# Kernel optimization log

Hardware: AMD Instinct MI355X
Metric: run time of the kernel (lower is better)

## Reference

```python
import jax, jax.numpy as jnp
import numpy as np

B, S, H, NH, L, FF, V, T = 16, 256, 768, 12, 12, 3072, 30522, 9
DH = H // NH
LN_EPS = 1e-12


def _ln(x, g, b):
    m = jnp.mean(x, axis=-1, keepdims=True)
    v = jnp.mean((x - m) ** 2, axis=-1, keepdims=True)
    return (x - m) * jax.lax.rsqrt(v + LN_EPS) * g + b


def setup_inputs():
    key = jax.random.key(0)
    ks = jax.random.split(key, 20)
    n = lambda i, shape: jax.random.normal(ks[i], shape, jnp.float32) * 0.02
    lengths = jax.random.randint(ks[0], (B,), S // 2, S + 1)
    attention_mask = (jnp.arange(S)[None, :] < lengths[:, None]).astype(jnp.int32)
    return {
        "input_ids": jax.random.randint(ks[1], (B, S), 0, V),
        "attention_mask": attention_mask,
        "labels": jax.random.randint(ks[2], (B, S), 0, T),
        "word_emb": n(3, (V, H)),
        "pos_emb": n(4, (512, H)),
        "type_emb": n(5, (2, H)),
        "emb_g": jnp.ones((H,), jnp.float32), "emb_b": jnp.zeros((H,), jnp.float32),
        "lWq": n(6, (L, H, H)), "lbq": jnp.zeros((L, H), jnp.float32),
        "lWk": n(7, (L, H, H)), "lbk": jnp.zeros((L, H), jnp.float32),
        "lWv": n(8, (L, H, H)), "lbv": jnp.zeros((L, H), jnp.float32),
        "lWo": n(9, (L, H, H)), "lbo": jnp.zeros((L, H), jnp.float32),
        "lg1": jnp.ones((L, H), jnp.float32), "lb1": jnp.zeros((L, H), jnp.float32),
        "lWi": n(10, (L, H, FF)), "lbi": jnp.zeros((L, FF), jnp.float32),
        "lWf": n(11, (L, FF, H)), "lbf": jnp.zeros((L, H), jnp.float32),
        "lg2": jnp.ones((L, H), jnp.float32), "lb2": jnp.zeros((L, H), jnp.float32),
        "cls_W": n(12, (H, T)), "cls_b": jnp.zeros((T,), jnp.float32),
        "crf_start": jax.random.uniform(ks[13], (T,), jnp.float32, -0.1, 0.1),
        "crf_end": jax.random.uniform(ks[14], (T,), jnp.float32, -0.1, 0.1),
        "crf_trans": jax.random.uniform(ks[15], (T, T), jnp.float32, -0.1, 0.1),
    }


def _encoder(input_ids, attention_mask, word_emb, pos_emb, type_emb, emb_g, emb_b, layer_stack, cls_W, cls_b):
    x = word_emb[input_ids] + pos_emb[:S][None] + type_emb[0][None, None]  # [B,S,H]
    x = _ln(x, emb_g, emb_b)
    bias = (1.0 - attention_mask.astype(jnp.float32))[:, None, None, :] * -1e9  # [B,1,1,S]
    scale = 1.0 / np.sqrt(DH).astype(np.float32)

    def layer(h, p):
        Wq, bq, Wk, bk, Wv, bv, Wo, bo, g1, b1, Wi, bi, Wf, bf, g2, b2 = p
        q = (h @ Wq + bq).reshape(B, S, NH, DH)
        k = (h @ Wk + bk).reshape(B, S, NH, DH)
        v = (h @ Wv + bv).reshape(B, S, NH, DH)
        att = jax.nn.softmax(jnp.einsum('bqhd,bkhd->bhqk', q, k) * scale + bias, axis=-1)
        ctx = jnp.einsum('bhqk,bkhd->bqhd', att, v).reshape(B, S, H)
        h = _ln(h + ctx @ Wo + bo, g1, b1)
        ff = jax.nn.gelu(h @ Wi + bi, approximate=False) @ Wf + bf
        h = _ln(h + ff, g2, b2)
        return h, None

    x, _ = jax.lax.scan(layer, x, layer_stack)
    return x @ cls_W + cls_b  # [B,S,T]


def _crf_llh(em, tg, m, start, end, trans):
    # pytorch-crf forward, reduction='sum'. em [B,Lc,T], tg [B,Lc] int, m [B,Lc] bool
    mf = m.astype(em.dtype)
    em_sc = jnp.take_along_axis(em, tg[..., None], axis=-1)[..., 0]  # [B,Lc]
    tr_sc = trans[tg[:, :-1], tg[:, 1:]]                             # [B,Lc-1]
    num = start[tg[:, 0]] + em_sc[:, 0] + jnp.sum(mf[:, 1:] * (tr_sc + em_sc[:, 1:]), axis=1)
    seq_ends = jnp.sum(m.astype(jnp.int32), axis=1) - 1
    last_tag = jnp.take_along_axis(tg, seq_ends[:, None], axis=1)[:, 0]
    num = num + end[last_tag]

    def step(score, xs):
        em_t, m_t = xs
        nxt = jax.nn.logsumexp(score[:, :, None] + trans[None] + em_t[:, None, :], axis=1)
        return jnp.where(m_t[:, None], nxt, score), None

    score0 = start[None] + em[:, 0]
    score, _ = jax.lax.scan(step, score0, (em[:, 1:].transpose(1, 0, 2), m[:, 1:].transpose(1, 0)))
    den = jax.nn.logsumexp(score + end[None], axis=1)
    return jnp.sum(num - den)


def _viterbi(em, start, end, trans):
    # decode over the FULL sequence with all-ones mask (matches crf.decode(logits))
    def step(score, em_t):
        cand = score[:, :, None] + trans[None] + em_t[:, None, :]  # [B,T,T]
        return jnp.max(cand, axis=1), jnp.argmax(cand, axis=1)

    score0 = start[None] + em[:, 0]
    score, hist = jax.lax.scan(step, score0, em[:, 1:].transpose(1, 0, 2))  # hist [S-1,B,T]
    last = jnp.argmax(score + end[None], axis=1)  # [B]

    def back(tag, h):
        prev = jnp.take_along_axis(h, tag[:, None], axis=1)[:, 0]
        return prev, prev

    _, rev = jax.lax.scan(back, last, hist, reverse=True)  # rev[i] = tag at time i, i in [0,S-2]
    tags = jnp.concatenate([rev.transpose(1, 0), last[:, None]], axis=1)  # [B,S]
    return tags.astype(jnp.float32)


def reference(input_ids, attention_mask, labels, word_emb, pos_emb, type_emb, emb_g, emb_b,
              lWq, lbq, lWk, lbk, lWv, lbv, lWo, lbo, lg1, lb1, lWi, lbi, lWf, lbf, lg2, lb2,
              cls_W, cls_b, crf_start, crf_end, crf_trans):
    layer_stack = (lWq, lbq, lWk, lbk, lWv, lbv, lWo, lbo, lg1, lb1, lWi, lbi, lWf, lbf, lg2, lb2)
    logits = _encoder(input_ids, attention_mask, word_emb, pos_emb, type_emb, emb_g, emb_b, layer_stack, cls_W, cls_b)
    str_lens = jnp.sum(attention_mask, axis=-1)
    pos = jnp.arange(S)[None, :]
    mask = attention_mask.astype(bool) & (pos > 0) & (pos != (str_lens - 1)[:, None])
    tags_in = jnp.where(mask, labels, jnp.zeros_like(labels))
    loss = -_crf_llh(logits[:, 1:], tags_in[:, 1:], mask[:, 1:], crf_start, crf_end, crf_trans)
    tags = _viterbi(logits, crf_start, crf_end, crf_trans)
    return (loss, tags)
```

## Files before the change

### kernel.cpp

```cpp
#include <hip/hip_runtime.h>

#define B_ 16
#define S_ 256
#define H_ 768
#define NH_ 12
#define DH_ 64
#define L_ 12
#define FF_ 3072
#define T_ 9
#define NTOK (B_*S_)

#define AS1 __attribute__((address_space(1)))
#define AS3 __attribute__((address_space(3)))

typedef __attribute__((ext_vector_type(8))) short bfrag;
typedef __attribute__((ext_vector_type(8))) unsigned short us8;
typedef __attribute__((ext_vector_type(4))) float f4;

#define LOG2E_ 1.4426950408889634f
#define LN2_   0.6931471805599453f

__device__ inline unsigned short f2bf(float x) {
    unsigned u = __builtin_bit_cast(unsigned, x);
    return (unsigned short)((u + 0x7fffu + ((u >> 16) & 1u)) >> 16);
}
__device__ inline float bf2f(unsigned short h) {
    unsigned u = ((unsigned)h) << 16;
    return __builtin_bit_cast(float, u);
}
__device__ inline void pack8(const float* v, us8& h, us8& l) {
    #pragma unroll
    for (int j = 0; j < 8; j++) {
        unsigned short hh = f2bf(v[j]);
        h[j] = hh;
        l[j] = f2bf(v[j] - bf2f(hh));
    }
}

__global__ __launch_bounds__(256) void k_conv_w(
    const float* __restrict__ Wq, const float* __restrict__ Wk,
    const float* __restrict__ Wv, const float* __restrict__ Wo,
    const float* __restrict__ Wi, const float* __restrict__ Wf,
    const float* __restrict__ bq, const float* __restrict__ bk, const float* __restrict__ bv,
    float* __restrict__ qkvbias, unsigned short* __restrict__ Wpk)
{
    int bid = blockIdx.x;
    int tid = threadIdx.x;
    if (bid == 0) {
        for (int i = tid; i < 3 * H_; i += 256)
            qkvbias[i] = (i < H_) ? bq[i] : (i < 2 * H_) ? bk[i - H_] : bv[i - 2 * H_];
    }
    const float* src; int Kd, Nd; size_t doff; int t;
    if (bid < 576)       { int m = bid / 144; src = (m == 0) ? Wq : (m == 1) ? Wk : (m == 2) ? Wv : Wo;
                           Kd = H_; Nd = H_; doff = (size_t)m * 73728; t = bid % 144; }
    else if (bid < 1152) { src = Wi; Kd = H_; Nd = FF_; doff = 294912; t = bid - 576; }
    else                 { src = Wf; Kd = FF_; Nd = H_; doff = 589824; t = bid - 1152; }
    int ntn = Nd / 64;
    int tk = t / ntn, tn = t % ntn;
    int k0 = tk * 64, n0 = tn * 64;
    __shared__ float tile[64][65];
    int r = tid >> 6, c = tid & 63;
    #pragma unroll
    for (int i = 0; i < 16; i++)
        tile[r + i * 4][c] = src[(size_t)(k0 + r + i * 4) * Nd + n0 + c];
    __syncthreads();
    #pragma unroll
    for (int e = 0; e < 2; e++) {
        int item = tid * 2 + e;
        int nl = item >> 3, kb = item & 7;
        float v8[8];
        #pragma unroll
        for (int j = 0; j < 8; j++) v8[j] = tile[kb * 8 + j][nl];
        us8 h, l; pack8(v8, h, l);
        unsigned short* p = Wpk + (doff + (size_t)(n0 + nl) * (Kd / 8) + (k0 / 8 + kb)) * 16;
        *reinterpret_cast<us8*>(p) = h;
        *reinterpret_cast<us8*>(p + 8) = l;
    }
}

__global__ __launch_bounds__(128) void k_embed_ln(
    const int* __restrict__ ids, const float* __restrict__ wemb,
    const float* __restrict__ pemb, const float* __restrict__ temb,
    const float* __restrict__ g, const float* __restrict__ bb,
    unsigned short* __restrict__ out_pk)
{
    int tok = blockIdx.x;
    int s = tok & (S_ - 1);
    int id = ids[tok];
    int tid = threadIdx.x;
    bool act = tid < 96;
    int idx = tid * 8;
    float v8[8];
    float sum = 0.f;
    if (act) {
        const float4* w4 = reinterpret_cast<const float4*>(wemb + (size_t)id * H_ + idx);
        const float4* p4 = reinterpret_cast<const float4*>(pemb + (size_t)s * H_ + idx);
        const float4* t4 = reinterpret_cast<const float4*>(temb + idx);
        #pragma unroll
        for (int q = 0; q < 2; q++) {
            float4 a = w4[q], b = p4[q], c = t4[q];
            v8[q*4+0] = a.x + b.x + c.x; v8[q*4+1] = a.y + b.y + c.y;
            v8[q*4+2] = a.z + b.z + c.z; v8[q*4+3] = a.w + b.w + c.w;
        }
        #pragma unroll
        for (int j = 0; j < 8; j++) sum += v8[j];
    }
    __shared__ float wsum[2], wvar[2];
    #pragma unroll
    for (int o = 32; o > 0; o >>= 1) sum += __shfl_xor(sum, o);
    if ((tid & 63) == 0) wsum[tid >> 6] = sum;
    __syncthreads();
    float mean = (wsum[0] + wsum[1]) * (1.0f / H_);
    float vs = 0.f;
    if (act) {
        for (int j = 0; j < 8; j++) { float d = v8[j] - mean; vs += d * d; }
    }
    #pragma unroll
    for (int o = 32; o > 0; o >>= 1) vs += __shfl_xor(vs, o);
    if ((tid & 63) == 0) wvar[tid >> 6] = vs;
    __syncthreads();
    float inv = 1.0f / sqrtf((wvar[0] + wvar[1]) * (1.0f / H_) + 1e-12f);
    if (act) {
        float o8[8];
        #pragma unroll
        for (int j = 0; j < 8; j++) o8[j] = (v8[j] - mean) * inv * g[idx + j] + bb[idx + j];
        us8 h, l; pack8(o8, h, l);
        unsigned short* p = out_pk + ((size_t)tok * 96 + tid) * 16;
        *reinterpret_cast<us8*>(p) = h;
        *reinterpret_cast<us8*>(p + 8) = l;
    }
}

__global__ __launch_bounds__(128) void k_res_ln(
    const float* __restrict__ x, const float* __restrict__ g, const float* __restrict__ bb,
    unsigned short* __restrict__ h_pk)
{
    int tok = blockIdx.x;
    int tid = threadIdx.x;
    bool act = tid < 96;
    int idx = tid * 8;
    float v8[8];
    float sum = 0.f;
    unsigned short* p = h_pk + ((size_t)tok * 96 + tid) * 16;
    if (act) {
        const float4* x4 = reinterpret_cast<const float4*>(x + (size_t)tok * H_ + idx);
        us8 hi = *reinterpret_cast<const us8*>(p);
        us8 lo = *reinterpret_cast<const us8*>(p + 8);
        float4 a0 = x4[0], a1 = x4[1];
        float xs[8] = {a0.x, a0.y, a0.z, a0.w, a1.x, a1.y, a1.z, a1.w};
        #pragma unroll
        for (int j = 0; j < 8; j++) {
            v8[j] = xs[j] + bf2f(hi[j]) + bf2f(lo[j]);
            sum += v8[j];
        }
    }
    __shared__ float wsum[2], wvar[2];
    #pragma unroll
    for (int o = 32; o > 0; o >>= 1) sum += __shfl_xor(sum, o);
    if ((tid & 63) == 0) wsum[tid >> 6] = sum;
    __syncthreads();
    float mean = (wsum[0] + wsum[1]) * (1.0f / H_);
    float vs = 0.f;
    if (act) {
        for (int j = 0; j < 8; j++) { float d = v8[j] - mean; vs += d * d; }
    }
    #pragma unroll
    for (int o = 32; o > 0; o >>= 1) vs += __shfl_xor(vs, o);
    if ((tid & 63) == 0) wvar[tid >> 6] = vs;
    __syncthreads();
    float inv = 1.0f / sqrtf((wvar[0] + wvar[1]) * (1.0f / H_) + 1e-12f);
    if (act) {
        float o8[8];
        #pragma unroll
        for (int j = 0; j < 8; j++) o8[j] = (v8[j] - mean) * inv * g[idx + j] + bb[idx + j];
        us8 h, l; pack8(o8, h, l);
        *reinterpret_cast<us8*>(p) = h;
        *reinterpret_cast<us8*>(p + 8) = l;
    }
}

__global__ __launch_bounds__(256) void k_gemm_pk(
    const unsigned short* __restrict__ A, const unsigned short* __restrict__ Wp,
    const float* __restrict__ bias,
    float* __restrict__ C0, float* __restrict__ C1, float* __restrict__ C2, int cpb,
    unsigned short* __restrict__ Cpk,
    int M, int N, int K, int act, int cbx)
{
    constexpr int BUFSZ = 24576;
    __shared__ char smem[3 * BUFSZ];
    unsigned smb = (unsigned)(size_t)(void*)smem;

    int id = blockIdx.x;
    int xcd = id & 7;
    int rr = id >> 3;
    int by = (xcd >> 1) * 8 + rr / cbx;
    int bx = (xcd & 1) * cbx + rr % cbx;
    int m0 = by << 7, n0 = bx << 6;
    int Kb = K >> 3;
    int nst = Kb >> 2;
    int rowbytes = Kb * 32;

    int tid = threadIdx.x;
    int lane = tid & 63, wid = tid >> 6;
    int wm = wid >> 1, wn = wid & 1;
    int fr = lane & 15, fq = lane >> 4;

    f4 acc[4][2];
    #pragma unroll
    for (int i = 0; i < 4; i++)
        #pragma unroll
        for (int j = 0; j < 2; j++) acc[i][j] = (f4){0.f, 0.f, 0.f, 0.f};

    const char* agp[4];
    const char* bgp[2];
    #pragma unroll
    for (int i = 0; i < 4; i++) {
        int d = i * 4096 + tid * 16;
        int row = d >> 7;
        int colp = (d & 127) ^ ((row & 7) << 4);
        agp[i] = (const char*)A + (size_t)(m0 + row) * rowbytes + colp;
    }
    #pragma unroll
    for (int i = 0; i < 2; i++) {
        int d = i * 4096 + tid * 16;
        int row = d >> 7;
        int colp = (d & 127) ^ ((row & 7) << 4);
        bgp[i] = (const char*)Wp + (size_t)(n0 + row) * rowbytes + colp;
    }

    int afo[4], bfo[2];
    #pragma unroll
    for (int mi = 0; mi < 4; mi++) {
        int r = wm * 64 + mi * 16 + fr;
        afo[mi] = r * 128 + ((fq * 32) ^ ((r & 7) << 4));
    }
    #pragma unroll
    for (int ni = 0; ni < 2; ni++) {
        int rb = wn * 32 + ni * 16 + fr;
        bfo[ni] = 16384 + rb * 128 + ((fq * 32) ^ ((rb & 7) << 4));
    }

    auto issue = [&](int ks, unsigned boff) {
        size_t ko = (size_t)ks * 128;
        #pragma unroll
        for (int i = 0; i < 4; i++)
            __builtin_amdgcn_global_load_lds((const AS1 void*)(size_t)(agp[i] + ko),
                (AS3 void*)(unsigned)(smb + boff + i * 4096 + wid * 1024), 16, 0, 0);
        #pragma unroll
        for (int i = 0; i < 2; i++)
            __builtin_amdgcn_global_load_lds((const AS1 void*)(size_t)(bgp[i] + ko),
                (AS3 void*)(unsigned)(smb + boff + 16384 + i * 4096 + wid * 1024), 16, 0, 0);
    };

    issue(0, 0);
    if (nst > 1) issue(1, BUFSZ);
    unsigned c0 = 0, c1 = BUFSZ, c2 = 2 * BUFSZ;

    for (int ks = 0; ks < nst; ks++) {
        if (ks + 1 < nst) asm volatile("s_waitcnt vmcnt(6)" ::: "memory");
        else              asm volatile("s_waitcnt vmcnt(0)" ::: "memory");
        __builtin_amdgcn_s_barrier();
        __builtin_amdgcn_sched_barrier(0);
        if (ks + 2 < nst) issue(ks + 2, c2);

        const char* cbp = smem + c0;
        bfrag ah[4], al[4], bh[2], bl[2];
        #pragma unroll
        for (int mi = 0; mi < 4; mi++) {
            ah[mi] = *reinterpret_cast<const bfrag*>(cbp + afo[mi]);
            al[mi] = *reinterpret_cast<const bfrag*>(cbp + (afo[mi] ^ 16));
        }
        #pragma unroll
        for (int ni = 0; ni < 2; ni++) {
            bh[ni] = *reinterpret_cast<const bfrag*>(cbp + bfo[ni]);
            bl[ni] = *reinterpret_cast<const bfrag*>(cbp + (bfo[ni] ^ 16));
        }
        #pragma unroll
        for (int mi = 0; mi < 4; mi++) {
            #pragma unroll
            for (int ni = 0; ni < 2; ni++) {
                acc[mi][ni] = __builtin_amdgcn_mfma_f32_16x16x32_bf16(ah[mi], bh[ni], acc[mi][ni], 0, 0, 0);
                acc[mi][ni] = __builtin_amdgcn_mfma_f32_16x16x32_bf16(ah[mi], bl[ni], acc[mi][ni], 0, 0, 0);
                acc[mi][ni] = __builtin_amdgcn_mfma_f32_16x16x32_bf16(al[mi], bh[ni], acc[mi][ni], 0, 0, 0);
            }
        }
        unsigned t = c0; c0 = c1; c1 = c2; c2 = t;
    }

    if (act == 0) {
        #pragma unroll
        for (int mi = 0; mi < 4; mi++) {
            #pragma unroll
            for (int ni = 0; ni < 2; ni++) {
                int col = n0 + wn * 32 + ni * 16 + fr;
                float bv = bias[col];
                int buf = col / cpb;
                float* Cp = (buf == 0) ? C0 : (buf == 1) ? C1 : C2;
                int cc = col - buf * cpb;
                #pragma unroll
                for (int r = 0; r < 4; r++) {
                    int row = m0 + wm * 64 + mi * 16 + fq * 4 + r;
                    Cp[(size_t)row * cpb + cc] = acc[mi][ni][r] + bv;
                }
            }
        }
    } else {
        __syncthreads();
        float* ebuf = (float*)(smem + wid * 2432);
        int Nb = N >> 3;
        #pragma unroll
        for (int mi = 0; mi < 4; mi++) {
            #pragma unroll
            for (int ni = 0; ni < 2; ni++) {
                int col = n0 + wn * 32 + ni * 16 + fr;
                float bv = bias[col];
                #pragma unroll
                for (int r = 0; r < 4; r++) {
                    float v = acc[mi][ni][r] + bv;
                    v = 0.5f * v * (1.0f + erff(v * 0.70710678118654752f));
                    ebuf[(fq * 4 + r) * 38 + ni * 16 + fr] = v;
                }
            }
            int row16 = lane >> 2, kb = lane & 3;
            float v8[8];
            #pragma unroll
            for (int j = 0; j < 8; j++) v8[j] = ebuf[row16 * 38 + kb * 8 + j];
            us8 h, l; pack8(v8, h, l);
            int grow = m0 + wm * 64 + mi * 16 + row16;
            int gcb = ((n0 + wn * 32) >> 3) + kb;
            unsigned short* p = Cpk + ((size_t)grow * Nb + gcb) * 16;
            *reinterpret_cast<us8*>(p) = h;
            *reinterpret_cast<us8*>(p + 8) = l;
        }
    }
}

#define SM_KH 0
#define SM_KL 5632
#define SM_VH 11264
#define SM_VL 16384
#define SM_PH 21504
#define SM_PL 26624
__global__ __launch_bounds__(256) void k_attn_fused(
    const float* __restrict__ Q, const float* __restrict__ Kb,
    const float* __restrict__ V, const int* __restrict__ amask,
    unsigned short* __restrict__ ctx_pk)
{
    __shared__ char smem[31744];
    unsigned short* KhS = (unsigned short*)(smem + SM_KH);
    unsigned short* KlS = (unsigned short*)(smem + SM_KL);
    unsigned short* VhS = (unsigned short*)(smem + SM_VH);
    unsigned short* VlS = (unsigned short*)(smem + SM_VL);
    unsigned short* PhS = (unsigned short*)(smem + SM_PH);
    unsigned short* PlS = (unsigned short*)(smem + SM_PL);

    int idx = blockIdx.x;
    int qt = idx & 3;
    int hd = (idx >> 2) % NH_;
    int b = idx / (4 * NH_);
    int tid = threadIdx.x;
    int lane = tid & 63, wid = tid >> 6;
    int fr = lane & 15, fq = lane >> 4;

    int q0 = qt * 64 + wid * 16;

    bfrag qh[2], ql[2];
    {
        const float* qbase = Q + ((size_t)(b * S_ + q0 + fr)) * H_ + hd * DH_;
        #pragma unroll
        for (int ks = 0; ks < 2; ks++) {
            const float4* p = reinterpret_cast<const float4*>(qbase + ks * 32 + fq * 8);
            float4 v0 = p[0], v1 = p[1];
            float vv[8] = {v0.x, v0.y, v0.z, v0.w, v1.x, v1.y, v1.z, v1.w};
            #pragma unroll
            for (int j = 0; j < 8; j++) {
                unsigned short h = f2bf(vv[j]);
                qh[ks][j] = (short)h;
                ql[ks][j] = (short)f2bf(vv[j] - bf2f(h));
            }
        }
    }

    f4 o[4];
    #pragma unroll
    for (int i = 0; i < 4; i++) o[i] = (f4){0.f, 0.f, 0.f, 0.f};
    float m[4], l[4];
    #pragma unroll
    for (int r = 0; r < 4; r++) { m[r] = -3e38f; l[r] = 0.f; }

    int kvrow = tid >> 3;
    int dbase = (tid & 7) * 8;

    for (int t = 0; t < 8; t++) {
        {
            const float* src = Kb + ((size_t)(b * S_ + t * 32 + kvrow)) * H_ + hd * DH_ + dbase;
            float4 a4 = reinterpret_cast<const float4*>(src)[0];
            float4 b4 = reinterpret_cast<const float4*>(src)[1];
            float vv[8] = {a4.x, a4.y, a4.z, a4.w, b4.x, b4.y, b4.z, b4.w};
            us8 h, l2;
            #pragma unroll
            for (int j = 0; j < 8; j++) {
                unsigned short hh = f2bf(vv[j]);
                h[j] = hh; l2[j] = f2bf(vv[j] - bf2f(hh));
            }
            *reinterpret_cast<us8*>(&KhS[kvrow * 88 + dbase]) = h;
            *reinterpret_cast<us8*>(&KlS[kvrow * 88 + dbase]) = l2;
        }
        {
            const float* src = V + ((size_t)(b * S_ + t * 32 + kvrow)) * H_ + hd * DH_ + dbase;
            float4 a4 = reinterpret_cast<const float4*>(src)[0];
            float4 b4 = reinterpret_cast<const float4*>(src)[1];
            float vv[8] = {a4.x, a4.y, a4.z, a4.w, b4.x, b4.y, b4.z, b4.w};
            #pragma unroll
            for (int j = 0; j < 8; j++) {
                unsigned short h = f2bf(vv[j]);
                VhS[(dbase + j) * 40 + kvrow] = h;
                VlS[(dbase + j) * 40 + kvrow] = f2bf(vv[j] - bf2f(h));
            }
        }
        __syncthreads();

        f4 s0 = (f4){0.f,0.f,0.f,0.f}, s1 = (f4){0.f,0.f,0.f,0.f};
        #pragma unroll
        for (int ks = 0; ks < 2; ks++) {
            bfrag kbh0 = *reinterpret_cast<const bfrag*>(&KhS[fr * 88 + ks * 32 + fq * 8]);
            bfrag kbl0 = *reinterpret_cast<const bfrag*>(&KlS[fr * 88 + ks * 32 + fq * 8]);
            bfrag kbh1 = *reinterpret_cast<const bfrag*>(&KhS[(16 + fr) * 88 + ks * 32 + fq * 8]);
            bfrag kbl1 = *reinterpret_cast<const bfrag*>(&KlS[(16 + fr) * 88 + ks * 32 + fq * 8]);
            s0 = __builtin_amdgcn_mfma_f32_16x16x32_bf16(qh[ks], kbh0, s0, 0, 0, 0);
            s0 = __builtin_amdgcn_mfma_f32_16x16x32_bf16(qh[ks], kbl0, s0, 0, 0, 0);
            s0 = __builtin_amdgcn_mfma_f32_16x16x32_bf16(ql[ks], kbh0, s0, 0, 0, 0);
            s1 = __builtin_amdgcn_mfma_f32_16x16x32_bf16(qh[ks], kbh1, s1, 0, 0, 0);
            s1 = __builtin_amdgcn_mfma_f32_16x16x32_bf16(qh[ks], kbl1, s1, 0, 0, 0);
            s1 = __builtin_amdgcn_mfma_f32_16x16x32_bf16(ql[ks], kbh1, s1, 0, 0, 0);
        }

        float cb0 = (amask[b * S_ + t * 32 + fr] == 0) ? -1e9f : 0.f;
        float cb1 = (amask[b * S_ + t * 32 + 16 + fr] == 0) ? -1e9f : 0.f;
        float sc0[4], sc1[4], fct[4], pr0[4], pr1[4];
        #pragma unroll
        for (int r = 0; r < 4; r++) {
            sc0[r] = s0[r] * 0.125f + cb0;
            sc1[r] = s1[r] * 0.125f + cb1;
            float tm = fmaxf(sc0[r], sc1[r]);
            #pragma unroll
            for (int od = 1; od < 16; od <<= 1) tm = fmaxf(tm, __shfl_xor(tm, od));
            float mn = fmaxf(m[r], tm);
            fct[r] = expf(m[r] - mn);
            pr0[r] = expf(sc0[r] - mn);
            pr1[r] = expf(sc1[r] - mn);
            float rs = pr0[r] + pr1[r];
            #pragma unroll
            for (int od = 1; od < 16; od <<= 1) rs += __shfl_xor(rs, od);
            l[r] = l[r] * fct[r] + rs;
            m[r] = mn;
        }
        #pragma unroll
        for (int ci = 0; ci < 4; ci++)
            #pragma unroll
            for (int r = 0; r < 4; r++) o[ci][r] *= fct[r];

        #pragma unroll
        for (int r = 0; r < 4; r++) {
            int row = fq * 4 + r;
            unsigned short h0 = f2bf(pr0[r]);
            PhS[wid * 640 + row * 40 + fr] = h0;
            PlS[wid * 640 + row * 40 + fr] = f2bf(pr0[r] - bf2f(h0));
            unsigned short h1 = f2bf(pr1[r]);
            PhS[wid * 640 + row * 40 + 16 + fr] = h1;
            PlS[wid * 640 + row * 40 + 16 + fr] = f2bf(pr1[r] - bf2f(h1));
        }

        bfrag pah = *reinterpret_cast<const bfrag*>(&PhS[wid * 640 + fr * 40 + fq * 8]);
        bfrag pal = *reinterpret_cast<const bfrag*>(&PlS[wid * 640 + fr * 40 + fq * 8]);
        #pragma unroll
        for (int ci = 0; ci < 4; ci++) {
            bfrag vbh = *reinterpret_cast<const bfrag*>(&VhS[(ci * 16 + fr) * 40 + fq * 8]);
            bfrag vbl = *reinterpret_cast<const bfrag*>(&VlS[(ci * 16 + fr) * 40 + fq * 8]);
            o[ci] = __builtin_amdgcn_mfma_f32_16x16x32_bf16(pah, vbh, o[ci], 0, 0, 0);
            o[ci] = __builtin_amdgcn_mfma_f32_16x16x32_bf16(pah, vbl, o[ci], 0, 0, 0);
            o[ci] = __builtin_amdgcn_mfma_f32_16x16x32_bf16(pal, vbh, o[ci], 0, 0, 0);
        }
        __syncthreads();
    }

    __syncthreads();
    float* eb = (float*)smem + wid * 1088;
    #pragma unroll
    for (int r = 0; r < 4; r++) {
        float inv = 1.0f / l[r];
        #pragma unroll
        for (int ci = 0; ci < 4; ci++)
            eb[(fq * 4 + r) * 68 + ci * 16 + fr] = o[ci][r] * inv;
    }
    __syncthreads();
    #pragma unroll
    for (int e = 0; e < 2; e++) {
        int item = lane * 2 + e;
        int row16 = item >> 3, kb = item & 7;
        float v8[8];
        #pragma unroll
        for (int j = 0; j < 8; j++) v8[j] = eb[row16 * 68 + kb * 8 + j];
        us8 h, l2; pack8(v8, h, l2);
        int grow = b * S_ + q0 + row16;
        int gcb = hd * 8 + kb;
        unsigned short* p = ctx_pk + ((size_t)grow * 96 + gcb) * 16;
        *reinterpret_cast<us8*>(p) = h;
        *reinterpret_cast<us8*>(p + 8) = l2;
    }
}

__global__ __launch_bounds__(64) void k_classifier(
    const unsigned short* __restrict__ Hpk, const float* __restrict__ Wc,
    const float* __restrict__ bc, float* __restrict__ logits)
{
    int tok = blockIdx.x;
    int lane = threadIdx.x;
    float acc[T_];
    #pragma unroll
    for (int j = 0; j < T_; j++) acc[j] = 0.f;
    for (int kb = lane; kb < 96; kb += 64) {
        const unsigned short* p = Hpk + ((size_t)tok * 96 + kb) * 16;
        us8 hi = *reinterpret_cast<const us8*>(p);
        us8 lo = *reinterpret_cast<const us8*>(p + 8);
        #pragma unroll
        for (int e = 0; e < 8; e++) {
            float hv = bf2f(hi[e]) + bf2f(lo[e]);
            const float* wr = Wc + (size_t)(kb * 8 + e) * T_;
            #pragma unroll
            for (int j = 0; j < T_; j++) acc[j] = fmaf(hv, wr[j], acc[j]);
        }
    }
    #pragma unroll
    for (int j = 0; j < T_; j++) {
        float v = acc[j];
        for (int o = 32; o > 0; o >>= 1) v += __shfl_down(v, o);
        if (lane == 0) logits[(size_t)tok * T_ + j] = v + bc[j];
    }
}

__global__ __launch_bounds__(256) void k_crf_vit(
    const float* __restrict__ logits, const int* __restrict__ amask,
    const int* __restrict__ labels, const float* __restrict__ start,
    const float* __restrict__ endv, const float* __restrict__ trans,
    float* __restrict__ out)
{
    int blk = blockIdx.x;
    int tid = threadIdx.x;
    if (blk == 0) {
        __shared__ float res[B_];
        int lane = tid & 63;
        int bb = (tid >> 6) * 4 + (lane >> 4);
        int sj = lane & 15;
        int lb = lane & 48;

        int cnt = 0;
        for (int s = sj; s < S_; s += 16) cnt += amask[bb * S_ + s];
        #pragma unroll
        for (int o = 8; o > 0; o >>= 1) cnt += __shfl_xor(cnt, o);
        int len = cnt;
        int lim = len - 1;

        float num = 0.f;
        for (int s = 2 + sj; s < S_; s += 16) {
            if (s < lim) {
                int tp = labels[bb * S_ + s - 1];
                int tc = labels[bb * S_ + s];
                num += trans[tp * T_ + tc] + logits[((size_t)(bb * S_ + s)) * T_ + tc];
            }
        }
        #pragma unroll
        for (int o = 8; o > 0; o >>= 1) num += __shfl_xor(num, o);
        int tg1 = labels[bb * S_ + 1];
        num += start[tg1] + logits[((size_t)(bb * S_ + 1)) * T_ + tg1];
        num += endv[labels[bb * S_ + (len - 2)]];

        float tc9[T_];
        #pragma unroll
        for (int i = 0; i < T_; i++) tc9[i] = (sj < T_) ? trans[i * T_ + sj] * LOG2E_ : 0.f;
        float score = (sj < T_) ? (start[sj] + logits[((size_t)(bb * S_ + 1)) * T_ + sj]) * LOG2E_ : 0.f;
        float base = 0.f;
        const float* embase = logits + (size_t)bb * S_ * T_ + sj;
        float emb[8];
        #pragma unroll
        for (int c = 0; c < 8; c++) emb[c] = (sj < T_) ? embase[(2 + c) * T_] : 0.f;
        for (int s0 = 2; s0 < S_; s0 += 8) {
            #pragma unroll
            for (int c = 0; c < 8; c++) {
                int s = s0 + c;
                if (s < S_) {
                    float em = emb[c];
                    emb[c] = (sj < T_ && s + 8 < S_) ? embase[(size_t)(s + 8) * T_] : 0.f;
                    float si[T_];
                    #pragma unroll
                    for (int i = 0; i < T_; i++) si[i] = __shfl(score, lb + i);
                    float e2[T_];
                    #pragma unroll
                    for (int i = 0; i < T_; i++) e2[i] = exp2f(si[i] + tc9[i]);
                    float s01 = e2[0] + e2[1], s23 = e2[2] + e2[3];
                    float s45 = e2[4] + e2[5], s67 = e2[6] + e2[7];
                    float sum = ((s01 + s23) + (s45 + s67)) + e2[8];
                    float nsc = fmaf(em, LOG2E_, log2f(sum));
                    if (s < lim) score = nsc;
                }
            }
            float sh = __shfl(score, lb);
            score -= sh;
            base += sh;
        }
        float se = (sj < T_) ? score + endv[sj] * LOG2E_ : -1e30f;
        float fi[T_];
        #pragma unroll
        for (int i = 0; i < T_; i++) fi[i] = __shfl(se, lb + i);
        if (sj == 0) {
            float mx = -1e30f;
            #pragma unroll
            for (int i = 0; i < T_; i++) mx = fmaxf(mx, fi[i]);
            float sum = 0.f;
            #pragma unroll
            for (int i = 0; i < T_; i++) sum += exp2f(fi[i] - mx);
            res[bb] = (base + mx + log2f(sum)) * LN2_ - num;
        }
        __syncthreads();
        if (tid == 0) {
            float tot = 0.f;
            #pragma unroll
            for (int i = 0; i < B_; i++) tot += res[i];
            out[0] = tot;
        }
    } else {
        if (tid >= 64) return;
        int b = blk - 1;
        int j = tid;
        float* tags_out = out + 1;
        __shared__ unsigned char hist[S_ - 1][T_];
        float tc9[T_];
        #pragma unroll
        for (int i = 0; i < T_; i++) tc9[i] = (j < T_) ? trans[i * T_ + j] : 0.f;
        float score = (j < T_) ? start[j] + logits[((size_t)(b * S_)) * T_ + j] : -1e30f;
        const float* embase = logits + (size_t)b * S_ * T_ + j;
        float emb[8];
        #pragma unroll
        for (int c = 0; c < 8; c++) emb[c] = (j < T_) ? embase[(1 + c) * T_] : 0.f;
        for (int t0 = 1; t0 < S_; t0 += 8) {
            #pragma unroll
            for (int c = 0; c < 8; c++) {
                int t = t0 + c;
                if (t < S_) {
                    float em = emb[c];
                    emb[c] = (j < T_ && t + 8 < S_) ? embase[(size_t)(t + 8) * T_] : 0.f;
                    float si[T_];
                    #pragma unroll
                    for (int i = 0; i < T_; i++) si[i] = __shfl(score, i);
                    float cv[T_];
                    #pragma unroll
                    for (int i = 0; i < T_; i++) cv[i] = si[i] + tc9[i];
                    float v01 = cv[0]; int i01 = 0; if (cv[1] > v01) { v01 = cv[1]; i01 = 1; }
                    float v23 = cv[2]; int i23 = 2; if (cv[3] > v23) { v23 = cv[3]; i23 = 3; }
                    float v45 = cv[4]; int i45 = 4; if (cv[5] > v45) { v45 = cv[5]; i45 = 5; }
                    float v67 = cv[6]; int i67 = 6; if (cv[7] > v67) { v67 = cv[7]; i67 = 7; }
                    float v03 = v01; int i03 = i01; if (v23 > v03) { v03 = v23; i03 = i23; }
                    float v47 = v45; int i47 = i45; if (v67 > v47) { v47 = v67; i47 = i67; }
                    float v07 = v03; int i07 = i03; if (v47 > v07) { v07 = v47; i07 = i47; }
                    float best = v07; int bi = i07; if (cv[8] > best) { best = cv[8]; bi = 8; }
                    if (j < T_) {
                        hist[t - 1][j] = (unsigned char)bi;
                        score = best + em;
                    }
                }
            }
        }
        float se = (j < T_) ? score + endv[j] : -1e30f;
        float fi[T_];
        #pragma unroll
        for (int i = 0; i < T_; i++) fi[i] = __shfl(se, i);
        if (j == 0) {
            float best = -1e30f; int last = 0;
            #pragma unroll
            for (int i = 0; i < T_; i++) if (fi[i] > best) { best = fi[i]; last = i; }
            tags_out[b * S_ + (S_ - 1)] = (float)last;
            int cur = last;
            for (int t = S_ - 2; t >= 0; t--) {
                cur = hist[t][cur];
                tags_out[b * S_ + t] = (float)cur;
            }
        }
    }
}

extern "C" void kernel_launch(void* const* d_in, const int* in_sizes, int n_in,
                              void* d_out, int out_size, void* d_ws, size_t ws_size,
                              hipStream_t stream)
{
    const int*   input_ids = (const int*)d_in[0];
    const int*   amask     = (const int*)d_in[1];
    const int*   labels    = (const int*)d_in[2];
    const float* word_emb  = (const float*)d_in[3];
    const float* pos_emb   = (const float*)d_in[4];
    const float* type_emb  = (const float*)d_in[5];
    const float* emb_g     = (const float*)d_in[6];
    const float* emb_b     = (const float*)d_in[7];
    const float* lWq = (const float*)d_in[8];
    const float* lbq = (const float*)d_in[9];
    const float* lWk = (const float*)d_in[10];
    const float* lbk = (const float*)d_in[11];
    const float* lWv = (const float*)d_in[12];
    const float* lbv = (const float*)d_in[13];
    const float* lWo = (const float*)d_in[14];
    const float* lbo = (const float*)d_in[15];
    const float* lg1 = (const float*)d_in[16];
    const float* lb1 = (const float*)d_in[17];
    const float* lWi = (const float*)d_in[18];
    const float* lbi = (const float*)d_in[19];
    const float* lWf = (const float*)d_in[20];
    const float* lbf = (const float*)d_in[21];
    const float* lg2 = (const float*)d_in[22];
    const float* lb2 = (const float*)d_in[23];
    const float* cls_W = (const float*)d_in[24];
    const float* cls_b = (const float*)d_in[25];
    const float* crf_start = (const float*)d_in[26];
    const float* crf_end   = (const float*)d_in[27];
    const float* crf_trans = (const float*)d_in[28];

    float* out = (float*)d_out;
    float* ws = (float*)d_ws;

    const size_t NH32 = (size_t)NTOK * H_;
    float* h_pk_f  = ws + NH32;
    float* q       = ws + 2 * NH32;
    float* kbuf    = ws + 3 * NH32;
    float* v       = ws + 4 * NH32;
    float* ctxpk_f = ws + 5 * NH32;
    float* tmp     = ws + 6 * NH32;
    float* Wpk_f   = ws + 7 * NH32;
    float* qkvbias = Wpk_f + 7077888;
    float* logits  = qkvbias + 3 * H_;

    unsigned short* h_pk   = (unsigned short*)h_pk_f;
    unsigned short* ctx_pk = (unsigned short*)ctxpk_f;
    unsigned short* Wpk    = (unsigned short*)Wpk_f;
    unsigned short* big_pk = (unsigned short*)q;

    k_embed_ln<<<NTOK, 128, 0, stream>>>(input_ids, word_emb, pos_emb, type_emb, emb_g, emb_b, h_pk);

    const size_t WOFF_O = 221184, WOFF_I = 294912, WOFF_F = 589824;

    for (int l = 0; l < L_; l++) {
        k_conv_w<<<1728, 256, 0, stream>>>(
            lWq + (size_t)l * H_ * H_, lWk + (size_t)l * H_ * H_,
            lWv + (size_t)l * H_ * H_, lWo + (size_t)l * H_ * H_,
            lWi + (size_t)l * H_ * FF_, lWf + (size_t)l * FF_ * H_,
            lbq + (size_t)l * H_, lbk + (size_t)l * H_, lbv + (size_t)l * H_,
            qkvbias, Wpk);

        k_gemm_pk<<<1152, 256, 0, stream>>>(h_pk, Wpk, qkvbias,
            q, kbuf, v, H_, nullptr, NTOK, 3 * H_, H_, 0, 18);

        k_attn_fused<<<B_ * NH_ * 4, 256, 0, stream>>>(q, kbuf, v, amask, ctx_pk);

        k_gemm_pk<<<384, 256, 0, stream>>>(ctx_pk, Wpk + WOFF_O * 16, lbo + (size_t)l * H_,
            tmp, tmp, tmp, H_, nullptr, NTOK, H_, H_, 0, 6);

        k_res_ln<<<NTOK, 128, 0, stream>>>(tmp, lg1 + (size_t)l * H_, lb1 + (size_t)l * H_, h_pk);

        k_gemm_pk<<<1536, 256, 0, stream>>>(h_pk, Wpk + WOFF_I * 16, lbi + (size_t)l * FF_,
            tmp, tmp, tmp, FF_, big_pk, NTOK, FF_, H_, 1, 24);

        k_gemm_pk<<<384, 256, 0, stream>>>(big_pk, Wpk + WOFF_F * 16, lbf + (size_t)l * H_,
            tmp, tmp, tmp, H_, nullptr, NTOK, H_, FF_, 0, 6);

        k_res_ln<<<NTOK, 128, 0, stream>>>(tmp, lg2 + (size_t)l * H_, lb2 + (size_t)l * H_, h_pk);
    }

    k_classifier<<<NTOK, 64, 0, stream>>>(h_pk, cls_W, cls_b, logits);
    k_crf_vit<<<1 + B_, 256, 0, stream>>>(logits, amask, labels, crf_start, crf_end, crf_trans, out);
}
```

Before: 3.570 ms.

## Add 256x128 GEMM tile kernel for QKV/FFN-up and stage CRF emissions in LDS

```diff
diff --git a/kernel.cpp b/kernel.cpp
--- a/kernel.cpp
+++ b/kernel.cpp
@@ -179,12 +179,171 @@
     }
 }
 
-__global__ __launch_bounds__(256) void k_gemm_pk(
+__global__ __launch_bounds__(512) void k_gemm_big(
     const unsigned short* __restrict__ A, const unsigned short* __restrict__ Wp,
     const float* __restrict__ bias,
     float* __restrict__ C0, float* __restrict__ C1, float* __restrict__ C2, int cpb,
     unsigned short* __restrict__ Cpk,
     int M, int N, int K, int act, int cbx)
+{
+    constexpr int BUFSZ = 49152;
+    __shared__ char smem[3 * BUFSZ];
+    unsigned smb = (unsigned)(size_t)(void*)smem;
+
+    int id = blockIdx.x;
+    int xcd = id & 7;
+    int rr = id >> 3;
+    int by = (xcd >> 1) * 4 + rr / cbx;
+    int bx = (xcd & 1) * cbx + rr % cbx;
+    int m0 = by << 8, n0 = bx << 7;
+    int Kb = K >> 3;
+    int nst = Kb >> 2;
+    int rowbytes = Kb * 32;
+
+    int tid = threadIdx.x;
+    int lane = tid & 63, wid = tid >> 6;
+    int wm = wid >> 1, wn = wid & 1;
+    int fr = lane & 15, fq = lane >> 4;
+
+    f4 acc[4][4];
+    #pragma unroll
+    for (int i = 0; i < 4; i++)
+        #pragma unroll
+        for (int j = 0; j < 4; j++) acc[i][j] = (f4){0.f, 0.f, 0.f, 0.f};
+
+    const char* agp[4];
+    const char* bgp[2];
+    #pragma unroll
+    for (int i = 0; i < 4; i++) {
+        int d = i * 8192 + tid * 16;
+        int row = d >> 7;
+        int colp = (d & 127) ^ ((row & 7) << 4);
+        agp[i] = (const char*)A + (size_t)(m0 + row) * rowbytes + colp;
+    }
+    #pragma unroll
+    for (int i = 0; i < 2; i++) {
+        int d = i * 8192 + tid * 16;
+        int row = d >> 7;
+        int colp = (d & 127) ^ ((row & 7) << 4);
+        bgp[i] = (const char*)Wp + (size_t)(n0 + row) * rowbytes + colp;
+    }
+
+    int afo[4], bfo[4];
+    #pragma unroll
+    for (int mi = 0; mi < 4; mi++) {
+        int r = wm * 64 + mi * 16 + fr;
+        afo[mi] = r * 128 + ((fq * 32) ^ ((r & 7) << 4));
+    }
+    #pragma unroll
+    for (int ni = 0; ni < 4; ni++) {
+        int rb = wn * 64 + ni * 16 + fr;
+        bfo[ni] = 32768 + rb * 128 + ((fq * 32) ^ ((rb & 7) << 4));
+    }
+
+    auto issue = [&](int ks, unsigned boff) {
+        size_t ko = (size_t)ks * 128;
+        #pragma unroll
+        for (int i = 0; i < 4; i++)
+            __builtin_amdgcn_global_load_lds((const AS1 void*)(size_t)(agp[i] + ko),
+                (AS3 void*)(unsigned)(smb + boff + i * 8192 + wid * 1024), 16, 0, 0);
+        #pragma unroll
+        for (int i = 0; i < 2; i++)
+            __builtin_amdgcn_global_load_lds((const AS1 void*)(size_t)(bgp[i] + ko),
+                (AS3 void*)(unsigned)(smb + boff + 32768 + i * 8192 + wid * 1024), 16, 0, 0);
+    };
+
+    issue(0, 0);
+    if (nst > 1) issue(1, BUFSZ);
+    unsigned c0 = 0, c1 = BUFSZ, c2 = 2 * BUFSZ;
+
+    for (int ks = 0; ks < nst; ks++) {
+        if (ks + 1 < nst) asm volatile("s_waitcnt vmcnt(6)" ::: "memory");
+        else              asm volatile("s_waitcnt vmcnt(0)" ::: "memory");
+        __builtin_amdgcn_s_barrier();
+        __builtin_amdgcn_sched_barrier(0);
+        if (ks + 2 < nst) issue(ks + 2, c2);
+
+        const char* cbp = smem + c0;
+        bfrag ah[4], al[4], bh[4], bl[4];
+        #pragma unroll
+        for (int mi = 0; mi < 4; mi++) {
+            ah[mi] = *reinterpret_cast<const bfrag*>(cbp + afo[mi]);
+            al[mi] = *reinterpret_cast<const bfrag*>(cbp + (afo[mi] ^ 16));
+        }
+        #pragma unroll
+        for (int ni = 0; ni < 4; ni++) {
+            bh[ni] = *reinterpret_cast<const bfrag*>(cbp + bfo[ni]);
+            bl[ni] = *reinterpret_cast<const bfrag*>(cbp + (bfo[ni] ^ 16));
+        }
+        #pragma unroll
+        for (int mi = 0; mi < 4; mi++) {
+            #pragma unroll
+            for (int ni = 0; ni < 4; ni++) {
+                acc[mi][ni] = __builtin_amdgcn_mfma_f32_16x16x32_bf16(ah[mi], bh[ni], acc[mi][ni], 0, 0, 0);
+                acc[mi][ni] = __builtin_amdgcn_mfma_f32_16x16x32_bf16(ah[mi], bl[ni], acc[mi][ni], 0, 0, 0);
+                acc[mi][ni] = __builtin_amdgcn_mfma_f32_16x16x32_bf16(al[mi], bh[ni], acc[mi][ni], 0, 0, 0);
+            }
+        }
+        unsigned t = c0; c0 = c1; c1 = c2; c2 = t;
+    }
+
+    if (act == 0) {
+        #pragma unroll
+        for (int mi = 0; mi < 4; mi++) {
+            #pragma unroll
+            for (int ni = 0; ni < 4; ni++) {
+                int col = n0 + wn * 64 + ni * 16 + fr;
+                float bv = bias[col];
+                int buf = col / cpb;
+                float* Cp = (buf == 0) ? C0 : (buf == 1) ? C1 : C2;
+                int cc = col - buf * cpb;
+                #pragma unroll
+                for (int r = 0; r < 4; r++) {
+                    int row = m0 + wm * 64 + mi * 16 + fq * 4 + r;
+                    Cp[(size_t)row * cpb + cc] = acc[mi][ni][r] + bv;
+                }
+            }
+        }
+    } else {
+        __syncthreads();
+        float* ebuf = (float*)(smem + wid * 4352);
+        int Nb = N >> 3;
+        #pragma unroll
+        for (int mi = 0; mi < 4; mi++) {
+            #pragma unroll
+            for (int ni = 0; ni < 4; ni++) {
+                int col = n0 + wn * 64 + ni * 16 + fr;
+                float bv = bias[col];
+                #pragma unroll
+                for (int r = 0; r < 4; r++) {
+                    float v = acc[mi][ni][r] + bv;
+                    v = 0.5f * v * (1.0f + erff(v * 0.70710678118654752f));
+                    ebuf[(fq * 4 + r) * 68 + ni * 16 + fr] = v;
+                }
+            }
+            #pragma unroll
+            for (int e = 0; e < 2; e++) {
+                int item = lane * 2 + e;
+                int row16 = item >> 3, kb = item & 7;
+                float v8[8];
+                #pragma unroll
+                for (int j = 0; j < 8; j++) v8[j] = ebuf[row16 * 68 + kb * 8 + j];
+                us8 h, l; pack8(v8, h, l);
+                int grow = m0 + wm * 64 + mi * 16 + row16;
+                int gcb = ((n0 + wn * 64) >> 3) + kb;
+                unsigned short* p = Cpk + ((size_t)grow * Nb + gcb) * 16;
+                *reinterpret_cast<us8*>(p) = h;
+                *reinterpret_cast<us8*>(p + 8) = l;
+            }
+        }
+    }
+}
+
+__global__ __launch_bounds__(256) void k_gemm_pk(
+    const unsigned short* __restrict__ A, const unsigned short* __restrict__ Wp,
+    const float* __restrict__ bias,
+    float* __restrict__ C0, int cpb,
+    int M, int N, int K, int cbx)
 {
     constexpr int BUFSZ = 24576;
     __shared__ char smem[3 * BUFSZ];
@@ -287,50 +446,17 @@
         unsigned t = c0; c0 = c1; c1 = c2; c2 = t;
     }
 
-    if (act == 0) {
-        #pragma unroll
-        for (int mi = 0; mi < 4; mi++) {
-            #pragma unroll
-            for (int ni = 0; ni < 2; ni++) {
-                int col = n0 + wn * 32 + ni * 16 + fr;
-                float bv = bias[col];
-                int buf = col / cpb;
-                float* Cp = (buf == 0) ? C0 : (buf == 1) ? C1 : C2;
-                int cc = col - buf * cpb;
-                #pragma unroll
-                for (int r = 0; r < 4; r++) {
-                    int row = m0 + wm * 64 + mi * 16 + fq * 4 + r;
-                    Cp[(size_t)row * cpb + cc] = acc[mi][ni][r] + bv;
-                }
-            }
-        }
-    } else {
-        __syncthreads();
-        float* ebuf = (float*)(smem + wid * 2432);
-        int Nb = N >> 3;
-        #pragma unroll
-        for (int mi = 0; mi < 4; mi++) {
-            #pragma unroll
-            for (int ni = 0; ni < 2; ni++) {
-                int col = n0 + wn * 32 + ni * 16 + fr;
-                float bv = bias[col];
-                #pragma unroll
-                for (int r = 0; r < 4; r++) {
-                    float v = acc[mi][ni][r] + bv;
-                    v = 0.5f * v * (1.0f + erff(v * 0.70710678118654752f));
-                    ebuf[(fq * 4 + r) * 38 + ni * 16 + fr] = v;
-                }
-            }
-            int row16 = lane >> 2, kb = lane & 3;
-            float v8[8];
-            #pragma unroll
-            for (int j = 0; j < 8; j++) v8[j] = ebuf[row16 * 38 + kb * 8 + j];
-            us8 h, l; pack8(v8, h, l);
-            int grow = m0 + wm * 64 + mi * 16 + row16;
-            int gcb = ((n0 + wn * 32) >> 3) + kb;
-            unsigned short* p = Cpk + ((size_t)grow * Nb + gcb) * 16;
-            *reinterpret_cast<us8*>(p) = h;
-            *reinterpret_cast<us8*>(p + 8) = l;
+    #pragma unroll
+    for (int mi = 0; mi < 4; mi++) {
+        #pragma unroll
+        for (int ni = 0; ni < 2; ni++) {
+            int col = n0 + wn * 32 + ni * 16 + fr;
+            float bv = bias[col];
+            #pragma unroll
+            for (int r = 0; r < 4; r++) {
+                int row = m0 + wm * 64 + mi * 16 + fq * 4 + r;
+                C0[(size_t)row * cpb + col] = acc[mi][ni][r] + bv;
+            }
         }
     }
 }
@@ -549,6 +675,7 @@
     int tid = threadIdx.x;
     if (blk == 0) {
         __shared__ float res[B_];
+        __shared__ float emS[B_ * 64 * T_];
         int lane = tid & 63;
         int bb = (tid >> 6) * 4 + (lane >> 4);
         int sj = lane & 15;
@@ -580,33 +707,42 @@
         for (int i = 0; i < T_; i++) tc9[i] = (sj < T_) ? trans[i * T_ + sj] * LOG2E_ : 0.f;
         float score = (sj < T_) ? (start[sj] + logits[((size_t)(bb * S_ + 1)) * T_ + sj]) * LOG2E_ : 0.f;
         float base = 0.f;
-        const float* embase = logits + (size_t)bb * S_ * T_ + sj;
-        float emb[8];
-        #pragma unroll
-        for (int c = 0; c < 8; c++) emb[c] = (sj < T_) ? embase[(2 + c) * T_] : 0.f;
-        for (int s0 = 2; s0 < S_; s0 += 8) {
-            #pragma unroll
-            for (int c = 0; c < 8; c++) {
-                int s = s0 + c;
-                if (s < S_) {
-                    float em = emb[c];
-                    emb[c] = (sj < T_ && s + 8 < S_) ? embase[(size_t)(s + 8) * T_] : 0.f;
-                    float si[T_];
-                    #pragma unroll
-                    for (int i = 0; i < T_; i++) si[i] = __shfl(score, lb + i);
-                    float e2[T_];
-                    #pragma unroll
-                    for (int i = 0; i < T_; i++) e2[i] = exp2f(si[i] + tc9[i]);
-                    float s01 = e2[0] + e2[1], s23 = e2[2] + e2[3];
-                    float s45 = e2[4] + e2[5], s67 = e2[6] + e2[7];
-                    float sum = ((s01 + s23) + (s45 + s67)) + e2[8];
-                    float nsc = fmaf(em, LOG2E_, log2f(sum));
-                    if (s < lim) score = nsc;
+
+        for (int ch = 0; ch < 4; ch++) {
+            int s0c = ch * 64;
+            __syncthreads();
+            #pragma unroll
+            for (int k = 0; k < 36; k++) {
+                int f = tid + k * 256;
+                int bbl = f / 576;
+                int rem = f - bbl * 576;
+                emS[f] = logits[(size_t)bbl * (S_ * T_) + s0c * T_ + rem];
+            }
+            __syncthreads();
+            const float* emc = emS + bb * 576 - (size_t)s0c * 9 + sj;
+            for (int s8 = s0c; s8 < s0c + 64; s8 += 8) {
+                #pragma unroll
+                for (int c = 0; c < 8; c++) {
+                    int s = s8 + c;
+                    if (s >= 2) {
+                        float em = (sj < T_) ? emc[(size_t)s * 9] : 0.f;
+                        float si[T_];
+                        #pragma unroll
+                        for (int i = 0; i < T_; i++) si[i] = __shfl(score, lb + i);
+                        float e2[T_];
+                        #pragma unroll
+                        for (int i = 0; i < T_; i++) e2[i] = exp2f(si[i] + tc9[i]);
+                        float s01 = e2[0] + e2[1], s23 = e2[2] + e2[3];
+                        float s45 = e2[4] + e2[5], s67 = e2[6] + e2[7];
+                        float sum = ((s01 + s23) + (s45 + s67)) + e2[8];
+                        float nsc = fmaf(em, LOG2E_, log2f(sum));
+                        if (s < lim) score = nsc;
+                    }
                 }
-            }
-            float sh = __shfl(score, lb);
-            score -= sh;
-            base += sh;
+                float sh = __shfl(score, lb);
+                score -= sh;
+                base += sh;
+            }
         }
         float se = (sj < T_) ? score + endv[sj] * LOG2E_ : -1e30f;
         float fi[T_];
@@ -629,26 +765,24 @@
             out[0] = tot;
         }
     } else {
+        int b = blk - 1;
+        __shared__ float emS2[S_ * T_];
+        __shared__ unsigned char hist[S_ - 1][T_];
+        for (int f = tid; f < S_ * T_; f += 256)
+            emS2[f] = logits[(size_t)b * (S_ * T_) + f];
+        __syncthreads();
         if (tid >= 64) return;
-        int b = blk - 1;
         int j = tid;
         float* tags_out = out + 1;
-        __shared__ unsigned char hist[S_ - 1][T_];
         float tc9[T_];
         #pragma unroll
         for (int i = 0; i < T_; i++) tc9[i] = (j < T_) ? trans[i * T_ + j] : 0.f;
-        float score = (j < T_) ? start[j] + logits[((size_t)(b * S_)) * T_ + j] : -1e30f;
-        const float* embase = logits + (size_t)b * S_ * T_ + j;
-        float emb[8];
-        #pragma unroll
-        for (int c = 0; c < 8; c++) emb[c] = (j < T_) ? embase[(1 + c) * T_] : 0.f;
+        float score = (j < T_) ? start[j] + emS2[j] : -1e30f;
         for (int t0 = 1; t0 < S_; t0 += 8) {
             #pragma unroll
             for (int c = 0; c < 8; c++) {
                 int t = t0 + c;
                 if (t < S_) {
-                    float em = emb[c];
-                    emb[c] = (j < T_ && t + 8 < S_) ? embase[(size_t)(t + 8) * T_] : 0.f;
                     float si[T_];
                     #pragma unroll
                     for (int i = 0; i < T_; i++) si[i] = __shfl(score, i);
@@ -665,7 +799,7 @@
                     float best = v07; int bi = i07; if (cv[8] > best) { best = cv[8]; bi = 8; }
                     if (j < T_) {
                         hist[t - 1][j] = (unsigned char)bi;
-                        score = best + em;
+                        score = best + emS2[t * 9 + j];
                     }
                 }
             }
@@ -753,21 +887,21 @@
             lbq + (size_t)l * H_, lbk + (size_t)l * H_, lbv + (size_t)l * H_,
             qkvbias, Wpk);
 
-        k_gemm_pk<<<1152, 256, 0, stream>>>(h_pk, Wpk, qkvbias,
-            q, kbuf, v, H_, nullptr, NTOK, 3 * H_, H_, 0, 18);
+        k_gemm_big<<<288, 512, 0, stream>>>(h_pk, Wpk, qkvbias,
+            q, kbuf, v, H_, nullptr, NTOK, 3 * H_, H_, 0, 9);
 
         k_attn_fused<<<B_ * NH_ * 4, 256, 0, stream>>>(q, kbuf, v, amask, ctx_pk);
 
         k_gemm_pk<<<384, 256, 0, stream>>>(ctx_pk, Wpk + WOFF_O * 16, lbo + (size_t)l * H_,
-            tmp, tmp, tmp, H_, nullptr, NTOK, H_, H_, 0, 6);
+            tmp, H_, NTOK, H_, H_, 6);
 
         k_res_ln<<<NTOK, 128, 0, stream>>>(tmp, lg1 + (size_t)l * H_, lb1 + (size_t)l * H_, h_pk);
 
-        k_gemm_pk<<<1536, 256, 0, stream>>>(h_pk, Wpk + WOFF_I * 16, lbi + (size_t)l * FF_,
-            tmp, tmp, tmp, FF_, big_pk, NTOK, FF_, H_, 1, 24);
+        k_gemm_big<<<384, 512, 0, stream>>>(h_pk, Wpk + WOFF_I * 16, lbi + (size_t)l * FF_,
+            tmp, tmp, tmp, FF_, big_pk, NTOK, FF_, H_, 1, 12);
 
         k_gemm_pk<<<384, 256, 0, stream>>>(big_pk, Wpk + WOFF_F * 16, lbf + (size_t)l * H_,
-            tmp, tmp, tmp, H_, nullptr, NTOK, H_, FF_, 0, 6);
+            tmp, H_, NTOK, H_, FF_, 6);
 
         k_res_ln<<<NTOK, 128, 0, stream>>>(tmp, lg2 + (size_t)l * H_, lb2 + (size_t)l * H_, h_pk);
     }
```

New measurement: 3.770 ms. +5.6%, slower.

## Stage CRF emissions in LDS and raise wave priority around GEMM MFMA block

Applied to the files above, without the earlier changes.

```diff
diff --git a/kernel.cpp b/kernel.cpp
--- a/kernel.cpp
+++ b/kernel.cpp
@@ -275,6 +275,7 @@
             bh[ni] = *reinterpret_cast<const bfrag*>(cbp + bfo[ni]);
             bl[ni] = *reinterpret_cast<const bfrag*>(cbp + (bfo[ni] ^ 16));
         }
+        __builtin_amdgcn_s_setprio(1);
         #pragma unroll
         for (int mi = 0; mi < 4; mi++) {
             #pragma unroll
@@ -284,6 +285,7 @@
                 acc[mi][ni] = __builtin_amdgcn_mfma_f32_16x16x32_bf16(al[mi], bh[ni], acc[mi][ni], 0, 0, 0);
             }
         }
+        __builtin_amdgcn_s_setprio(0);
         unsigned t = c0; c0 = c1; c1 = c2; c2 = t;
     }
 
@@ -549,6 +551,7 @@
     int tid = threadIdx.x;
     if (blk == 0) {
         __shared__ float res[B_];
+        __shared__ float emS[B_ * 64 * T_];
         int lane = tid & 63;
         int bb = (tid >> 6) * 4 + (lane >> 4);
         int sj = lane & 15;
@@ -580,33 +583,42 @@
         for (int i = 0; i < T_; i++) tc9[i] = (sj < T_) ? trans[i * T_ + sj] * LOG2E_ : 0.f;
         float score = (sj < T_) ? (start[sj] + logits[((size_t)(bb * S_ + 1)) * T_ + sj]) * LOG2E_ : 0.f;
         float base = 0.f;
-        const float* embase = logits + (size_t)bb * S_ * T_ + sj;
-        float emb[8];
-        #pragma unroll
-        for (int c = 0; c < 8; c++) emb[c] = (sj < T_) ? embase[(2 + c) * T_] : 0.f;
-        for (int s0 = 2; s0 < S_; s0 += 8) {
-            #pragma unroll
-            for (int c = 0; c < 8; c++) {
-                int s = s0 + c;
-                if (s < S_) {
-                    float em = emb[c];
-                    emb[c] = (sj < T_ && s + 8 < S_) ? embase[(size_t)(s + 8) * T_] : 0.f;
-                    float si[T_];
-                    #pragma unroll
-                    for (int i = 0; i < T_; i++) si[i] = __shfl(score, lb + i);
-                    float e2[T_];
-                    #pragma unroll
-                    for (int i = 0; i < T_; i++) e2[i] = exp2f(si[i] + tc9[i]);
-                    float s01 = e2[0] + e2[1], s23 = e2[2] + e2[3];
-                    float s45 = e2[4] + e2[5], s67 = e2[6] + e2[7];
-                    float sum = ((s01 + s23) + (s45 + s67)) + e2[8];
-                    float nsc = fmaf(em, LOG2E_, log2f(sum));
-                    if (s < lim) score = nsc;
+
+        for (int ch = 0; ch < 4; ch++) {
+            int s0c = ch * 64;
+            __syncthreads();
+            #pragma unroll
+            for (int k = 0; k < 36; k++) {
+                int f = tid + k * 256;
+                int bbl = f / 576;
+                int rem = f - bbl * 576;
+                emS[f] = logits[(size_t)bbl * (S_ * T_) + s0c * T_ + rem];
+            }
+            __syncthreads();
+            const float* emc = emS + bb * 576 - (size_t)s0c * 9 + sj;
+            for (int s8 = s0c; s8 < s0c + 64; s8 += 8) {
+                #pragma unroll
+                for (int c = 0; c < 8; c++) {
+                    int s = s8 + c;
+                    if (s >= 2) {
+                        float em = (sj < T_) ? emc[(size_t)s * 9] : 0.f;
+                        float si[T_];
+                        #pragma unroll
+                        for (int i = 0; i < T_; i++) si[i] = __shfl(score, lb + i);
+                        float e2[T_];
+                        #pragma unroll
+                        for (int i = 0; i < T_; i++) e2[i] = exp2f(si[i] + tc9[i]);
+                        float s01 = e2[0] + e2[1], s23 = e2[2] + e2[3];
+                        float s45 = e2[4] + e2[5], s67 = e2[6] + e2[7];
+                        float sum = ((s01 + s23) + (s45 + s67)) + e2[8];
+                        float nsc = fmaf(em, LOG2E_, log2f(sum));
+                        if (s < lim) score = nsc;
+                    }
                 }
-            }
-            float sh = __shfl(score, lb);
-            score -= sh;
-            base += sh;
+                float sh = __shfl(score, lb);
+                score -= sh;
+                base += sh;
+            }
         }
         float se = (sj < T_) ? score + endv[sj] * LOG2E_ : -1e30f;
         float fi[T_];
@@ -629,26 +641,24 @@
             out[0] = tot;
         }
     } else {
+        int b = blk - 1;
+        __shared__ float emS2[S_ * T_];
+        __shared__ unsigned char hist[S_ - 1][T_];
+        for (int f = tid; f < S_ * T_; f += 256)
+            emS2[f] = logits[(size_t)b * (S_ * T_) + f];
+        __syncthreads();
         if (tid >= 64) return;
-        int b = blk - 1;
         int j = tid;
         float* tags_out = out + 1;
-        __shared__ unsigned char hist[S_ - 1][T_];
         float tc9[T_];
         #pragma unroll
         for (int i = 0; i < T_; i++) tc9[i] = (j < T_) ? trans[i * T_ + j] : 0.f;
-        float score = (j < T_) ? start[j] + logits[((size_t)(b * S_)) * T_ + j] : -1e30f;
-        const float* embase = logits + (size_t)b * S_ * T_ + j;
-        float emb[8];
-        #pragma unroll
-        for (int c = 0; c < 8; c++) emb[c] = (j < T_) ? embase[(1 + c) * T_] : 0.f;
+        float score = (j < T_) ? start[j] + emS2[j] : -1e30f;
         for (int t0 = 1; t0 < S_; t0 += 8) {
             #pragma unroll
             for (int c = 0; c < 8; c++) {
                 int t = t0 + c;
                 if (t < S_) {
-                    float em = emb[c];
-                    emb[c] = (j < T_ && t + 8 < S_) ? embase[(size_t)(t + 8) * T_] : 0.f;
                     float si[T_];
                     #pragma unroll
                     for (int i = 0; i < T_; i++) si[i] = __shfl(score, i);
@@ -665,7 +675,7 @@
                     float best = v07; int bi = i07; if (cv[8] > best) { best = cv[8]; bi = 8; }
                     if (j < T_) {
                         hist[t - 1][j] = (unsigned char)bi;
-                        score = best + em;
+                        score = best + emS2[t * 9 + j];
                     }
                 }
             }
```

After: 3.608 ms. About the same (+1.0%).
